# Performance work log

Hardware: AMD Instinct MI355X
Metric: run time of the kernel (lower is better)

The kernel has to match this reference:

```python
import jax, jax.numpy as jnp
import numpy as np

B, L, D, H = 4, 2048, 2048, 16
HD = D // H
EPS = 1e-6


def _rope_tables(l, hd, base=10000.0):
    inv = 1.0 / (base ** (np.arange(0, hd, 2, dtype=np.float32) / hd))  # [hd/2]
    t = np.arange(l, dtype=np.float32)
    ang = np.outer(t, inv)  # [l, hd/2]
    return jnp.asarray(np.cos(ang)), jnp.asarray(np.sin(ang))


def setup_inputs() -> dict:
    key = jax.random.key(0)
    ks = jax.random.split(key, 8)
    cos, sin = _rope_tables(L, HD)
    s = 1.0 / np.sqrt(D)
    return {
        "x": jax.random.normal(ks[0], (B, L, D), jnp.float32),
        "freqs_cos": cos,
        "freqs_sin": sin,
        "Wqk": jax.random.normal(ks[1], (D, 2 * D), jnp.float32) * s,
        "Wv": jax.random.normal(ks[2], (D, D), jnp.float32) * s,
        "bv": jax.random.normal(ks[3], (D,), jnp.float32) * 0.02,
        "Wp": jax.random.normal(ks[4], (D, D), jnp.float32) * s,
        "bp": jax.random.normal(ks[5], (D,), jnp.float32) * 0.02,
        "qn_w": jnp.ones((HD,), jnp.float32),
        "kn_w": jnp.ones((HD,), jnp.float32),
    }


def _rmsnorm(x, w, eps=EPS):
    ms = jnp.mean(jnp.square(x), axis=-1, keepdims=True)
    return x * jax.lax.rsqrt(ms + eps) * w


def _rope(x, cos, sin):
    # x: [b,h,l,hd]; cos/sin: [l,hd/2]; interleaved (complex) rotation
    x1 = x[..., 0::2]
    x2 = x[..., 1::2]
    c = cos[None, None, :, :]
    s = sin[None, None, :, :]
    out = jnp.stack([x1 * c - x2 * s, x1 * s + x2 * c], axis=-1)
    return out.reshape(x.shape)


def reference(x, freqs_cos, freqs_sin, Wqk, Wv, bv, Wp, bp, qn_w, kn_w):
    b, l, d = x.shape
    qk = x @ Wqk  # [b,l,2d]
    q, k = jnp.split(qk, 2, axis=-1)
    v = x @ Wv + bv
    # [b,l,d] -> [b,h,l,hd]
    to_heads = lambda t: t.reshape(b, l, H, HD).transpose(0, 2, 1, 3)
    q, k, v = to_heads(q), to_heads(k), to_heads(v)
    q = _rmsnorm(q, qn_w)
    k = _rmsnorm(k, kn_w)
    q = _rope(q, freqs_cos, freqs_sin)
    k = _rope(k, freqs_cos, freqs_sin)
    scale = 1.0 / jnp.sqrt(jnp.asarray(HD, q.dtype))
    scores = jnp.einsum("bhqd,bhkd->bhqk", q, k) * scale
    causal = jnp.tril(jnp.ones((l, l), bool))
    scores = jnp.where(causal[None, None], scores, jnp.asarray(-1e30, scores.dtype))
    attn = jax.nn.softmax(scores, axis=-1)
    y = jnp.einsum("bhqk,bhkd->bhqd", attn, v)
    y = y.transpose(0, 2, 1, 3).reshape(b, l, d)
    return y @ Wp + bp
```

## Files before the change

### kernel.cpp

```cpp
#include <hip/hip_runtime.h>
#include <hip/hip_bf16.h>
#include <math.h>

#define B_  4
#define L_  2048
#define D_  2048
#define H_  16
#define HD_ 128
#define BH_ (B_*H_)
#define BL_ (B_*L_)

typedef __attribute__((ext_vector_type(4))) float  f32x4;
typedef __attribute__((ext_vector_type(8))) __bf16 bf16x8;

static __device__ __forceinline__ float bf2f(unsigned short u) {
    union { unsigned int i; float f; } v; v.i = ((unsigned int)u) << 16; return v.f;
}
static __device__ __forceinline__ unsigned short f2bf(float f) {
    union { float f; unsigned int i; } v; v.f = f;
    unsigned int x = v.i;
    return (unsigned short)((x + 0x7fffu + ((x >> 16) & 1u)) >> 16);
}

static __device__ __forceinline__ void gload16(const unsigned short* g, unsigned short* l) {
    __builtin_amdgcn_global_load_lds(
        (const __attribute__((address_space(1))) unsigned int*)(const void*)g,
        (__attribute__((address_space(3))) unsigned int*)(void*)l, 16, 0, 0);
}

__global__ __launch_bounds__(256) void k_f32_to_bf16(const float* __restrict__ s,
                                                     unsigned short* __restrict__ d, int n8) {
    int i = blockIdx.x * 256 + threadIdx.x;
    if (i >= n8) return;
    const float* p = s + (size_t)i * 8;
    float4 a = *(const float4*)p;
    float4 b = *(const float4*)(p + 4);
    union { bf16x8 v; unsigned short u[8]; } o;
    o.u[0]=f2bf(a.x); o.u[1]=f2bf(a.y); o.u[2]=f2bf(a.z); o.u[3]=f2bf(a.w);
    o.u[4]=f2bf(b.x); o.u[5]=f2bf(b.y); o.u[6]=f2bf(b.z); o.u[7]=f2bf(b.w);
    *(bf16x8*)(d + (size_t)i * 8) = o.v;
}

__global__ __launch_bounds__(256) void k_transpose_f2b(const float* __restrict__ src,
                                                       unsigned short* __restrict__ dst,
                                                       int R, int C, int dstStride) {
    __shared__ float tile[32][33];
    int tx = threadIdx.x & 31, ty = threadIdx.x >> 5;
    int c0 = blockIdx.x * 32, r0 = blockIdx.y * 32;
    #pragma unroll
    for (int i = 0; i < 32; i += 8)
        tile[ty + i][tx] = src[(size_t)(r0 + ty + i) * C + c0 + tx];
    __syncthreads();
    #pragma unroll
    for (int i = 0; i < 32; i += 8)
        dst[(size_t)(c0 + ty + i) * dstStride + r0 + tx] = f2bf(tile[tx][ty + i]);
}

__global__ __launch_bounds__(256) void k_transpose_v(const unsigned short* __restrict__ vb,
                                                     unsigned short* __restrict__ vT) {
    __shared__ unsigned short tile[32][33];
    int bh = blockIdx.z;
    int hd0 = blockIdx.x * 32, l0 = blockIdx.y * 32;
    int tx = threadIdx.x & 31, ty = threadIdx.x >> 5;
    const unsigned short* in = vb + (size_t)bh * L_ * HD_;
    unsigned short* out      = vT + (size_t)bh * L_ * HD_;
    #pragma unroll
    for (int i = 0; i < 32; i += 8)
        tile[ty + i][tx] = in[(size_t)(l0 + ty + i) * HD_ + hd0 + tx];
    __syncthreads();
    #pragma unroll
    for (int i = 0; i < 32; i += 8)
        out[(size_t)(hd0 + ty + i) * L_ + l0 + tx] = tile[tx][ty + i];
}


template<int MG, int NG>
static __device__ __forceinline__ void mfma_quad(const bf16x8 (&afr)[4][2],
                                                 const bf16x8 (&bfr)[2][2],
                                                 f32x4 (&acc)[8][4]) {
    #pragma unroll
    for (int mi = 0; mi < 4; ++mi)
        #pragma unroll
        for (int ni = 0; ni < 2; ++ni) {
            acc[MG*4+mi][NG*2+ni] = __builtin_amdgcn_mfma_f32_16x16x32_bf16(
                afr[mi][0], bfr[ni][0], acc[MG*4+mi][NG*2+ni], 0, 0, 0);
            acc[MG*4+mi][NG*2+ni] = __builtin_amdgcn_mfma_f32_16x16x32_bf16(
                afr[mi][1], bfr[ni][1], acc[MG*4+mi][NG*2+ni], 0, 0, 0);
        }
}

static __device__ __forceinline__ void ds_load_a(const unsigned short* u, int wm,
                                                 int l15, int l4, bf16x8 (&afr)[4][2]) {
    int sw = l15 & 7;
    #pragma unroll
    for (int mi = 0; mi < 4; ++mi) {
        int ro = (wm*64 + mi*16 + l15) * 64;
        afr[mi][0] = *(const bf16x8*)(u + ro + ((l4 ^ sw) << 3));
        afr[mi][1] = *(const bf16x8*)(u + ro + (((4 + l4) ^ sw) << 3));
    }
}

static __device__ __forceinline__ void ds_load_b(const unsigned short* u, int wn,
                                                 int l15, int l4, bf16x8 (&bfr)[2][2]) {
    int sw = l15 & 7;
    #pragma unroll
    for (int ni = 0; ni < 2; ++ni) {
        int ro = (wn*32 + ni*16 + l15) * 64;
        bfr[ni][0] = *(const bf16x8*)(u + ro + ((l4 ^ sw) << 3));
        bfr[ni][1] = *(const bf16x8*)(u + ro + (((4 + l4) ^ sw) << 3));
    }
}

#define STAGE_A_(c_, mg_, t_) do {                                                        \
    gload16(gA + (size_t)(((mg_)*64      ) * 2048) + (t_)*64, &Lds[c_][0][mg_][w*512]);   \
    gload16(gA + (size_t)(((mg_)*64 + 128) * 2048) + (t_)*64, &Lds[c_][0][mg_][4096 + w*512]); \
} while (0)
#define STAGE_B_(c_, ng_, t_) do {                                                        \
    gload16(gB + (size_t)(((ng_)*32 + ((w>>2)    )*64) * 2048) + (t_)*64, &Lds[c_][1][ng_][w*512]); \
    gload16(gB + (size_t)(((ng_)*32 + ((w>>2) + 2)*64) * 2048) + (t_)*64, &Lds[c_][1][ng_][4096 + w*512]); \
} while (0)
#define SB_() __builtin_amdgcn_sched_barrier(0)

template<int MODE>
__global__ __launch_bounds__(512, 2) void k_gemm(const unsigned short* __restrict__ A,
                                                 const unsigned short* __restrict__ Bt,
                                                 int M, int N, int K,
                                                 const float* __restrict__ bias,
                                                 unsigned short* __restrict__ qout,
                                                 unsigned short* __restrict__ kout,
                                                 unsigned short* __restrict__ vout,
                                                 float* __restrict__ fout) {
    (void)K;
    __shared__ __align__(16) unsigned short Lds[2][2][2][8192];
    const int tid = threadIdx.x;
    const int lane = tid & 63, w = tid >> 6;
    const int wm = w >> 2, wn = w & 3;
    const int l15 = lane & 15, l4 = lane >> 4;
    const int lsw = (lane & 7) ^ ((lane >> 3) & 7);

    int nwgx = gridDim.x;
    int bid = blockIdx.y * nwgx + blockIdx.x;
    int cpx = (nwgx * gridDim.y) >> 3;
    int sb = (bid & 7) * cpx + (bid >> 3);
    int n0 = (sb % nwgx) * 256, m0 = (sb / nwgx) * 256;

    const unsigned short* gA = A  + (size_t)(m0 + w*8 + (lane >> 3)) * 2048 + lsw*8;
    const unsigned short* gB = Bt + (size_t)(n0 + (w&3)*8 + (lane >> 3)) * 2048 + lsw*8;

    f32x4 acc[8][4] = {};
    bf16x8 afr[4][2], bf0[2][2], bf1[2][2];
    const int nt = 2048 / 64;

    STAGE_A_(0, 0, 0); STAGE_B_(0, 0, 0); STAGE_B_(0, 1, 0); STAGE_A_(0, 1, 0);
    STAGE_A_(1, 0, 1); STAGE_B_(1, 0, 1); STAGE_B_(1, 1, 1);
    asm volatile("s_waitcnt vmcnt(6)" ::: "memory");
    __builtin_amdgcn_s_barrier();

    for (int t = 0; t < nt; ++t) {
        const int c = t & 1, cn = c ^ 1;
        const bool h1 = (t + 1 < nt), h2 = (t + 2 < nt);

        ds_load_a(&Lds[c][0][0][0], wm, l15, l4, afr);
        ds_load_b(&Lds[c][1][0][0], wn, l15, l4, bf0);
        SB_();
        ds_load_b(&Lds[c][1][1][0], wn, l15, l4, bf1);
        SB_();
        if (h1) STAGE_A_(cn, 1, t + 1);
        __builtin_amdgcn_s_barrier();
        asm volatile("s_waitcnt lgkmcnt(4)" ::: "memory");
        SB_();
        __builtin_amdgcn_s_setprio(1);
        mfma_quad<0, 0>(afr, bf0, acc);
        __builtin_amdgcn_s_setprio(0);
        SB_();
        __builtin_amdgcn_s_barrier();

        asm volatile("s_waitcnt lgkmcnt(0)" ::: "memory");
        SB_();
        __builtin_amdgcn_s_setprio(1);
        mfma_quad<0, 1>(afr, bf1, acc);
        __builtin_amdgcn_s_setprio(0);
        SB_();
        ds_load_a(&Lds[c][0][1][0], wm, l15, l4, afr);
        SB_();
        if (h2) STAGE_A_(c, 0, t + 2);
        __builtin_amdgcn_s_barrier();

        if (h2) STAGE_B_(c, 0, t + 2);
        asm volatile("s_waitcnt lgkmcnt(0)" ::: "memory");
        SB_();
        __builtin_amdgcn_s_setprio(1);
        mfma_quad<1, 1>(afr, bf1, acc);
        __builtin_amdgcn_s_setprio(0);
        SB_();
        if (h2) STAGE_B_(c, 1, t + 2);
        __builtin_amdgcn_s_setprio(1);
        mfma_quad<1, 0>(afr, bf0, acc);
        __builtin_amdgcn_s_setprio(0);
        SB_();
        if (h2) asm volatile("s_waitcnt vmcnt(4)" ::: "memory");
        else    asm volatile("s_waitcnt vmcnt(0)" ::: "memory");
        __builtin_amdgcn_s_barrier();
    }

    #pragma unroll
    for (int mi = 0; mi < 8; ++mi) {
        #pragma unroll
        for (int ni = 0; ni < 4; ++ni) {
            int ncol = n0 + wn*64 + ni*16 + l15;
            #pragma unroll
            for (int j = 0; j < 4; ++j) {
                int m = m0 + wm*128 + mi*16 + l4*4 + j;
                float v = acc[mi][ni][j];
                if (MODE == 0) {
                    int b = m >> 11, l = m & 2047;
                    if (ncol < 2048) {
                        int h = ncol >> 7, hd = ncol & 127;
                        qout[((size_t)(b*H_ + h) * L_ + l) * HD_ + hd] = f2bf(v);
                    } else if (ncol < 4096) {
                        int cc = ncol - 2048, h = cc >> 7, hd = cc & 127;
                        kout[((size_t)(b*H_ + h) * L_ + l) * HD_ + hd] = f2bf(v);
                    } else {
                        int cc = ncol - 4096, h = cc >> 7, hd = cc & 127;
                        vout[((size_t)(b*H_ + h) * L_ + l) * HD_ + hd] = f2bf(v + bias[cc]);
                    }
                } else {
                    fout[(size_t)m * N + ncol] = v + bias[ncol];
                }
            }
        }
    }
}

__global__ __launch_bounds__(256) void k_normrope(unsigned short* __restrict__ qb,
                                                  unsigned short* __restrict__ kb,
                                                  const float* __restrict__ cosT,
                                                  const float* __restrict__ sinT,
                                                  const float* __restrict__ qw,
                                                  const float* __restrict__ kw) {
    int lane = threadIdx.x & 63;
    int row = blockIdx.x * 4 + (threadIdx.x >> 6);
    int isK = row >= BH_ * L_;
    unsigned short* buf = isK ? kb : qb;
    const float* w = isK ? kw : qw;
    int r = isK ? row - BH_ * L_ : row;
    int l = r & (L_ - 1);
    unsigned short* p = buf + (size_t)r * HD_ + lane * 2;
    ushort2 u = *(const ushort2*)p;
    float x1 = bf2f(u.x), x2 = bf2f(u.y);
    float ss = x1*x1 + x2*x2;
    #pragma unroll
    for (int off = 32; off; off >>= 1) ss += __shfl_xor(ss, off);
    float rs = rsqrtf(ss * (1.0f / 128.0f) + 1e-6f);
    float c = cosT[l * 64 + lane], s = sinT[l * 64 + lane];
    float y1 = x1 * rs * w[lane * 2];
    float y2 = x2 * rs * w[lane * 2 + 1];
    ushort2 o;
    o.x = f2bf(y1 * c - y2 * s);
    o.y = f2bf(y1 * s + y2 * c);
    *(ushort2*)p = o;
}

#define PLDT 72

__global__ __launch_bounds__(256) void k_attn(const unsigned short* __restrict__ qbuf,
                                              const unsigned short* __restrict__ kbuf,
                                              const unsigned short* __restrict__ vT,
                                              unsigned short* __restrict__ yb) {
    __shared__ __align__(16) unsigned short Ks[64 * 128];
    __shared__ __align__(16) unsigned short Vs[128 * 64];
    __shared__ __align__(16) unsigned short Ps[4][32 * PLDT];
    int tid = threadIdx.x, lane = tid & 63, w = tid >> 6;
    int l15 = lane & 15, l4 = lane >> 4;
    int qb = 15 - (blockIdx.x >> 6);
    int bh = blockIdx.x & 63;
    const unsigned short* Q  = qbuf + (size_t)bh * L_ * HD_;
    const unsigned short* Kp = kbuf + (size_t)bh * L_ * HD_;
    const unsigned short* Vp = vT   + (size_t)bh * L_ * HD_;
    int qr0 = qb * 128 + w * 32;

    bf16x8 qf[2][4];
    #pragma unroll
    for (int m = 0; m < 2; ++m)
        #pragma unroll
        for (int ks = 0; ks < 4; ++ks)
            qf[m][ks] = *(const bf16x8*)(Q + (size_t)(qr0 + m*16 + l15) * HD_ + ks*32 + l4*8);

    f32x4 accO[2][8] = {};
    f32x4 accW[2] = {};
    float mrow[2][4];
    #pragma unroll
    for (int m = 0; m < 2; ++m)
        #pragma unroll
        for (int j = 0; j < 4; ++j) mrow[m][j] = -1e30f;

    bf16x8 vones;
    #pragma unroll
    for (int i = 0; i < 8; ++i) vones[i] = (__bf16)1.0f;

    const float scale = 0.08838834764831845f;
    int nkt = 2 * qb + 2;

    for (int kt = 0; kt < nkt; ++kt) {
        int kbase = kt * 64;
        #pragma unroll
        for (int i = 0; i < 4; ++i) {
            int g = w * 4 + i;
            int kr = g * 4 + (lane >> 4);
            gload16(Kp + (size_t)(kbase + kr) * HD_ + (((lane & 15) ^ (kr & 15)) << 3),
                    Ks + g * 512);
            int vr = g * 8 + (lane >> 3);
            gload16(Vp + (size_t)vr * L_ + kbase + (((lane & 7) ^ (vr & 7)) << 3),
                    Vs + g * 512);
        }
        __syncthreads();

        if (kbase <= qr0 + 31) {
            f32x4 sf[2][4] = {};
            #pragma unroll
            for (int f = 0; f < 4; ++f)
                #pragma unroll
                for (int ks = 0; ks < 4; ++ks) {
                    bf16x8 kf = *(const bf16x8*)(Ks + (f*16 + l15) * 128 +
                                                 ((((ks*4) + l4) ^ l15) << 3));
                    sf[0][f] = __builtin_amdgcn_mfma_f32_16x16x32_bf16(qf[0][ks], kf, sf[0][f], 0, 0, 0);
                    sf[1][f] = __builtin_amdgcn_mfma_f32_16x16x32_bf16(qf[1][ks], kf, sf[1][f], 0, 0, 0);
                }

            #pragma unroll
            for (int m = 0; m < 2; ++m) {
                bool needmask = (kbase + 63 > qr0 + m*16);
                #pragma unroll
                for (int f = 0; f < 4; ++f)
                    #pragma unroll
                    for (int j = 0; j < 4; ++j) {
                        float s = sf[m][f][j] * scale;
                        if (needmask) {
                            int key  = kbase + f*16 + l15;
                            int qrow = qr0 + m*16 + l4*4 + j;
                            if (key > qrow) s = -1e30f;
                        }
                        sf[m][f][j] = s;
                    }
            }

            float mx[2][4];
            #pragma unroll
            for (int m = 0; m < 2; ++m)
                #pragma unroll
                for (int j = 0; j < 4; ++j) {
                    float v = fmaxf(fmaxf(sf[m][0][j], sf[m][1][j]),
                                    fmaxf(sf[m][2][j], sf[m][3][j]));
                    #pragma unroll
                    for (int off = 1; off < 16; off <<= 1) v = fmaxf(v, __shfl_xor(v, off));
                    mx[m][j] = v;
                }

            float drift = mx[0][0] - mrow[0][0];
            #pragma unroll
            for (int m = 0; m < 2; ++m)
                #pragma unroll
                for (int j = 0; j < 4; ++j) drift = fmaxf(drift, mx[m][j] - mrow[m][j]);
            if (!__all(drift <= 8.0f)) {
                #pragma unroll
                for (int m = 0; m < 2; ++m)
                    #pragma unroll
                    for (int j = 0; j < 4; ++j) {
                        float mnew = fmaxf(mrow[m][j], mx[m][j]);
                        float corr = __expf(mrow[m][j] - mnew);
                        mrow[m][j] = mnew;
                        accW[m][j] *= corr;
                        #pragma unroll
                        for (int cf = 0; cf < 8; ++cf) accO[m][cf][j] *= corr;
                    }
            }

            unsigned short* ps = Ps[w];
            #pragma unroll
            for (int m = 0; m < 2; ++m)
                #pragma unroll
                for (int f = 0; f < 4; ++f)
                    #pragma unroll
                    for (int j = 0; j < 4; ++j) {
                        float p = __expf(sf[m][f][j] - mrow[m][j]);
                        *(__bf16*)(ps + (m*16 + l4*4 + j) * PLDT + f*16 + l15) = (__bf16)p;
                    }

            #pragma unroll
            for (int ks = 0; ks < 2; ++ks) {
                bf16x8 pa0 = *(const bf16x8*)(ps + l15 * PLDT + ks*32 + l4*8);
                bf16x8 pa1 = *(const bf16x8*)(ps + (16 + l15) * PLDT + ks*32 + l4*8);
                #pragma unroll
                for (int cf = 0; cf < 8; ++cf) {
                    bf16x8 vf = *(const bf16x8*)(Vs + (cf*16 + l15) * 64 +
                                                 ((((ks*4) + l4) ^ (l15 & 7)) << 3));
                    accO[0][cf] = __builtin_amdgcn_mfma_f32_16x16x32_bf16(pa0, vf, accO[0][cf], 0, 0, 0);
                    accO[1][cf] = __builtin_amdgcn_mfma_f32_16x16x32_bf16(pa1, vf, accO[1][cf], 0, 0, 0);
                }
                accW[0] = __builtin_amdgcn_mfma_f32_16x16x32_bf16(pa0, vones, accW[0], 0, 0, 0);
                accW[1] = __builtin_amdgcn_mfma_f32_16x16x32_bf16(pa1, vones, accW[1], 0, 0, 0);
            }
        }
        __syncthreads();
    }

    int b = bh >> 4, h = bh & 15;
    #pragma unroll
    for (int m = 0; m < 2; ++m)
        #pragma unroll
        for (int cf = 0; cf < 8; ++cf)
            #pragma unroll
            for (int j = 0; j < 4; ++j) {
                int qrow = qr0 + m*16 + l4*4 + j;
                float o = accO[m][cf][j] / accW[m][j];
                yb[((size_t)(b * L_ + qrow)) * D_ + h*128 + cf*16 + l15] = f2bf(o);
            }
}

extern "C" void kernel_launch(void* const* d_in, const int* in_sizes, int n_in,
                              void* d_out, int out_size, void* d_ws, size_t ws_size,
                              hipStream_t stream) {
    const float* x    = (const float*)d_in[0];
    const float* fcos = (const float*)d_in[1];
    const float* fsin = (const float*)d_in[2];
    const float* Wqk  = (const float*)d_in[3];
    const float* Wv   = (const float*)d_in[4];
    const float* bv   = (const float*)d_in[5];
    const float* Wp   = (const float*)d_in[6];
    const float* bp   = (const float*)d_in[7];
    const float* qn_w = (const float*)d_in[8];
    const float* kn_w = (const float*)d_in[9];
    float* out = (float*)d_out;

    char* ws = (char*)d_ws;
    unsigned short* Wt   = (unsigned short*)(ws);
    unsigned short* Wpt  = (unsigned short*)(ws + 25165824);
    unsigned short* xb   = (unsigned short*)(ws + 33554432);
    unsigned short* qbuf = (unsigned short*)(ws + 67108864);
    unsigned short* kbuf = (unsigned short*)(ws + 100663296);
    unsigned short* vbuf = (unsigned short*)(ws + 134217728);
    unsigned short* vTb  = (unsigned short*)(ws + 167772160);
    unsigned short* yb   = xb;

    k_f32_to_bf16<<<8192, 256, 0, stream>>>(x, xb, BL_ * D_ / 8);
    k_transpose_f2b<<<dim3(128, 64), 256, 0, stream>>>(Wqk, Wt, 2048, 4096, 2048);
    k_transpose_f2b<<<dim3(64, 64),  256, 0, stream>>>(Wv,  Wt + (size_t)4096 * 2048, 2048, 2048, 2048);
    k_transpose_f2b<<<dim3(64, 64),  256, 0, stream>>>(Wp,  Wpt, 2048, 2048, 2048);

    k_gemm<0><<<dim3(24, 32), 512, 0, stream>>>(xb, Wt, BL_, 6144, 2048, bv,
                                                qbuf, kbuf, vbuf, nullptr);
    k_normrope<<<2 * BH_ * L_ / 4, 256, 0, stream>>>(qbuf, kbuf, fcos, fsin, qn_w, kn_w);
    k_transpose_v<<<dim3(4, 64, 64), 256, 0, stream>>>(vbuf, vTb);
    k_attn<<<BH_ * (L_ / 128), 256, 0, stream>>>(qbuf, kbuf, vTb, yb);
    k_gemm<1><<<dim3(8, 32), 512, 0, stream>>>(yb, Wpt, BL_, 2048, 2048, bp,
                                               nullptr, nullptr, nullptr, out);
}
```

Measured before the change: 561.2 us.

## Pipeline K/V tile loads in attention and fold softmax scale into Q

Splits the attention loop so the next K tile is fetched asynchronously while the P·V product runs, replacing __syncthreads with explicit vmcnt waits and raw barriers. Folds the 1/sqrt(hd)*log2(e) factor into Q during norm/rope, so the kernel drops the per-score multiply and uses exp2f. The rescale threshold is raised to match the log2 domain. This adds more barriers per iteration and relies on hand-counted vmcnt values, which could cause races if the count is wrong.

```diff
diff --git a/kernel.cpp b/kernel.cpp
--- a/kernel.cpp
+++ b/kernel.cpp
@@ -72,7 +72,6 @@
     for (int i = 0; i < 32; i += 8)
         out[(size_t)(hd0 + ty + i) * L_ + l0 + tx] = tile[tx][ty + i];
 }
-
 
 template<int MG, int NG>
 static __device__ __forceinline__ void mfma_quad(const bf16x8 (&afr)[4][2],
@@ -238,6 +237,7 @@
                                                   const float* __restrict__ sinT,
                                                   const float* __restrict__ qw,
                                                   const float* __restrict__ kw) {
+    const float QSCL = 0.08838834764831845f * 1.4426950408889634f;
     int lane = threadIdx.x & 63;
     int row = blockIdx.x * 4 + (threadIdx.x >> 6);
     int isK = row >= BH_ * L_;
@@ -252,6 +252,7 @@
     #pragma unroll
     for (int off = 32; off; off >>= 1) ss += __shfl_xor(ss, off);
     float rs = rsqrtf(ss * (1.0f / 128.0f) + 1e-6f);
+    rs *= isK ? 1.0f : QSCL;
     float c = cosT[l * 64 + lane], s = sinT[l * 64 + lane];
     float y1 = x1 * rs * w[lane * 2];
     float y2 = x2 * rs * w[lane * 2 + 1];
@@ -298,24 +299,32 @@
     #pragma unroll
     for (int i = 0; i < 8; ++i) vones[i] = (__bf16)1.0f;
 
-    const float scale = 0.08838834764831845f;
     int nkt = 2 * qb + 2;
+
+    #pragma unroll
+    for (int i = 0; i < 4; ++i) {
+        int g = w * 4 + i;
+        int kr = g * 4 + l4;
+        gload16(Kp + (size_t)kr * HD_ + (((lane & 15) ^ (kr & 15)) << 3), Ks + g * 512);
+    }
+    SB_();
 
     for (int kt = 0; kt < nkt; ++kt) {
         int kbase = kt * 64;
+        bool compute = (kbase <= qr0 + 31);
+
         #pragma unroll
         for (int i = 0; i < 4; ++i) {
             int g = w * 4 + i;
-            int kr = g * 4 + (lane >> 4);
-            gload16(Kp + (size_t)(kbase + kr) * HD_ + (((lane & 15) ^ (kr & 15)) << 3),
-                    Ks + g * 512);
             int vr = g * 8 + (lane >> 3);
             gload16(Vp + (size_t)vr * L_ + kbase + (((lane & 7) ^ (vr & 7)) << 3),
                     Vs + g * 512);
         }
-        __syncthreads();
-
-        if (kbase <= qr0 + 31) {
+        SB_();
+        asm volatile("s_waitcnt vmcnt(4)" ::: "memory");
+        __builtin_amdgcn_s_barrier();
+
+        if (compute) {
             f32x4 sf[2][4] = {};
             #pragma unroll
             for (int f = 0; f < 4; ++f)
@@ -330,18 +339,15 @@
             #pragma unroll
             for (int m = 0; m < 2; ++m) {
                 bool needmask = (kbase + 63 > qr0 + m*16);
-                #pragma unroll
-                for (int f = 0; f < 4; ++f)
+                if (needmask)
                     #pragma unroll
-                    for (int j = 0; j < 4; ++j) {
-                        float s = sf[m][f][j] * scale;
-                        if (needmask) {
+                    for (int f = 0; f < 4; ++f)
+                        #pragma unroll
+                        for (int j = 0; j < 4; ++j) {
                             int key  = kbase + f*16 + l15;
                             int qrow = qr0 + m*16 + l4*4 + j;
-                            if (key > qrow) s = -1e30f;
+                            if (key > qrow) sf[m][f][j] = -1e30f;
                         }
-                        sf[m][f][j] = s;
-                    }
             }
 
             float mx[2][4];
@@ -361,13 +367,13 @@
             for (int m = 0; m < 2; ++m)
                 #pragma unroll
                 for (int j = 0; j < 4; ++j) drift = fmaxf(drift, mx[m][j] - mrow[m][j]);
-            if (!__all(drift <= 8.0f)) {
+            if (!__all(drift <= 11.5f)) {
                 #pragma unroll
                 for (int m = 0; m < 2; ++m)
                     #pragma unroll
                     for (int j = 0; j < 4; ++j) {
                         float mnew = fmaxf(mrow[m][j], mx[m][j]);
-                        float corr = __expf(mrow[m][j] - mnew);
+                        float corr = exp2f(mrow[m][j] - mnew);
                         mrow[m][j] = mnew;
                         accW[m][j] *= corr;
                         #pragma unroll
@@ -382,10 +388,30 @@
                 for (int f = 0; f < 4; ++f)
                     #pragma unroll
                     for (int j = 0; j < 4; ++j) {
-                        float p = __expf(sf[m][f][j] - mrow[m][j]);
+                        float p = exp2f(sf[m][f][j] - mrow[m][j]);
                         *(__bf16*)(ps + (m*16 + l4*4 + j) * PLDT + f*16 + l15) = (__bf16)p;
                     }
-
+        }
+        __builtin_amdgcn_s_barrier();
+
+        if (kt + 1 < nkt) {
+            int kb2 = kbase + 64;
+            #pragma unroll
+            for (int i = 0; i < 4; ++i) {
+                int g = w * 4 + i;
+                int kr = g * 4 + l4;
+                gload16(Kp + (size_t)(kb2 + kr) * HD_ + (((lane & 15) ^ (kr & 15)) << 3),
+                        Ks + g * 512);
+            }
+            SB_();
+            asm volatile("s_waitcnt vmcnt(4)" ::: "memory");
+        } else {
+            asm volatile("s_waitcnt vmcnt(0)" ::: "memory");
+        }
+        __builtin_amdgcn_s_barrier();
+
+        if (compute) {
+            unsigned short* ps = Ps[w];
             #pragma unroll
             for (int ks = 0; ks < 2; ++ks) {
                 bf16x8 pa0 = *(const bf16x8*)(ps + l15 * PLDT + ks*32 + l4*8);
@@ -401,7 +427,7 @@
                 accW[1] = __builtin_amdgcn_mfma_f32_16x16x32_bf16(pa1, vones, accW[1], 0, 0, 0);
             }
         }
-        __syncthreads();
+        __builtin_amdgcn_s_barrier();
     }
 
     int b = bh >> 4, h = bh & 15;
```

New measurement: 588.8 us. 1.05x slower.
